# Kernel tuning notes

Measured on AMD Instinct MI355X. Metric: run time of the kernel, lower is better.

The kernel has to match this reference:

```python
import jax, jax.numpy as jnp
import numpy as np
import math

D_MODEL = 2048
D_STATE = 16
DT_RANK = math.ceil(D_MODEL / 16)  # 128
DT_MIN, DT_MAX, DT_INIT_FLOOR = 0.001, 0.1, 1e-4


def setup_inputs() -> dict:
    key = jax.random.key(0)
    k1, k2, k3, k4 = jax.random.split(key, 4)
    B, L = 4, 2048
    hidden_states = jax.random.normal(k1, (B, L, D_MODEL), dtype=jnp.float32)
    # x_proj: Linear(d_model -> dt_rank + 2*d_state), no bias
    fan_in = D_MODEL
    bound = 1.0 / math.sqrt(fan_in)
    x_proj_w = jax.random.uniform(k2, (DT_RANK + 2 * D_STATE, D_MODEL),
                                  minval=-bound, maxval=bound, dtype=jnp.float32)
    # dt_proj: Linear(dt_rank -> d_model) with special init
    dt_init_std = DT_RANK ** (-0.5)
    dt_proj_w = jax.random.uniform(k3, (D_MODEL, DT_RANK),
                                   minval=-dt_init_std, maxval=dt_init_std,
                                   dtype=jnp.float32)
    dt = jnp.exp(jax.random.uniform(k4, (D_MODEL,), dtype=jnp.float32)
                 * (math.log(DT_MAX) - math.log(DT_MIN)) + math.log(DT_MIN))
    dt = jnp.clip(dt, DT_INIT_FLOOR, None)
    dt_proj_b = dt + jnp.log(-jnp.expm1(-dt))  # inverse softplus
    # A_log: log(1..d_state) broadcast to (d_model, d_state)
    A_log = jnp.log(jnp.broadcast_to(jnp.arange(1, D_STATE + 1, dtype=jnp.float32),
                                     (D_MODEL, D_STATE)))
    D = jnp.ones((D_MODEL,), dtype=jnp.float32)
    return {"hidden_states": hidden_states, "x_proj_w": x_proj_w,
            "dt_proj_w": dt_proj_w, "dt_proj_b": dt_proj_b,
            "A_log": A_log, "D": D}


def _selective_scan(u, delta, A, Bmat, Cmat, D):
    # u, delta: (b, l, d); A: (d, n); Bmat, Cmat: (b, l, n); D: (d,)
    b, l, d = u.shape
    n = A.shape[1]

    def step(h, inp):
        u_t, delta_t, B_t, C_t = inp  # (b,d), (b,d), (b,n), (b,n)
        dA = jnp.exp(delta_t[:, :, None] * A)                 # (b,d,n)
        dBu = (delta_t * u_t)[:, :, None] * B_t[:, None, :]   # (b,d,n)
        h = dA * h + dBu
        y_t = jnp.einsum('bdn,bn->bd', h, C_t)
        return h, y_t

    h0 = jnp.zeros((b, d, n), dtype=u.dtype)
    xs = (jnp.swapaxes(u, 0, 1), jnp.swapaxes(delta, 0, 1),
          jnp.swapaxes(Bmat, 0, 1), jnp.swapaxes(Cmat, 0, 1))
    _, ys = jax.lax.scan(step, h0, xs)      # ys: (l, b, d)
    y = jnp.swapaxes(ys, 0, 1)               # (b, l, d)
    return y + u * D


def reference(hidden_states, x_proj_w, dt_proj_w, dt_proj_b, A_log, D):
    A = -jnp.exp(A_log)                                   # (d, n)
    x_dbl = hidden_states @ x_proj_w.T                    # (b, l, R+2n)
    dt_r = x_dbl[..., :DT_RANK]
    Bmat = x_dbl[..., DT_RANK:DT_RANK + D_STATE]          # (b, l, n)
    Cmat = x_dbl[..., DT_RANK + D_STATE:]                 # (b, l, n)
    dt = dt_r @ dt_proj_w.T                               # (b, l, d)
    delta = jax.nn.softplus(dt + dt_proj_b)               # fused delta_bias + softplus
    return _selective_scan(hidden_states, delta, A, Bmat, Cmat, D)
```

## Files before the change

### kernel.cpp

```cpp
#include <hip/hip_runtime.h>
#include <hip/hip_bf16.h>
#include <math.h>


#define DM   2048
#define DS   16
#define RNK  128
#define XDW  160
#define LSEQ 2048
#define NB   4
#define MTOT (NB * LSEQ)

#define G1_BM   64
#define G1_BK   32
#define G1_KS   8
#define G1_KPB  (DM / G1_KS)
#define G1_NCH  (G1_KPB / G1_BK)
#define XDBL_ELEMS ((size_t)MTOT * XDW)

typedef __attribute__((ext_vector_type(8))) unsigned short u16x8;
__global__ __launch_bounds__(256) void f32_to_bf16_kern(const float* __restrict__ in,
                                                        unsigned short* __restrict__ out) {
    const size_t i = ((size_t)blockIdx.x * 256 + threadIdx.x) * 8;
    const float4 v0 = *(const float4*)(in + i);
    const float4 v1 = *(const float4*)(in + i + 4);
    const float vv[8] = {v0.x, v0.y, v0.z, v0.w, v1.x, v1.y, v1.z, v1.w};
    u16x8 o;
    #pragma unroll
    for (int j = 0; j < 8; ++j) {
        __hip_bfloat16 h = __float2bfloat16(vv[j]);
        o[j] = *(unsigned short*)&h;
    }
    *(u16x8*)(out + i) = o;
}

typedef __attribute__((ext_vector_type(8))) short bf16x8;
typedef __attribute__((ext_vector_type(4))) float f32x4;

__global__ __launch_bounds__(256) void gemm1_mfma(const unsigned short* __restrict__ hsb,
                                                  const unsigned short* __restrict__ w1b,
                                                  float* __restrict__ out) {
    const int w  = threadIdx.x >> 6;
    const int l  = threadIdx.x & 63;
    const int m0 = blockIdx.x * G1_BM + w * 16;
    const int k0 = blockIdx.y * G1_KPB;
    const int lr = l & 15;
    const int lk = (l >> 4) * 8;

    f32x4 acc[10];
    #pragma unroll
    for (int j = 0; j < 10; ++j) acc[j] = (f32x4){0.f, 0.f, 0.f, 0.f};

    const unsigned short* ap = hsb + (size_t)(m0 + lr) * DM + k0 + lk;
    const unsigned short* bp = w1b + (size_t)lr * DM + k0 + lk;
    for (int ks = 0; ks < G1_KPB / 32; ++ks) {
        const bf16x8 a = *(const bf16x8*)(ap + ks * 32);
        #pragma unroll
        for (int j = 0; j < 10; ++j) {
            const bf16x8 b = *(const bf16x8*)(bp + (size_t)j * 16 * DM + ks * 32);
            acc[j] = __builtin_amdgcn_mfma_f32_16x16x32_bf16(a, b, acc[j], 0, 0, 0);
        }
    }
    float* op = out + (size_t)blockIdx.y * XDBL_ELEMS;
    #pragma unroll
    for (int j = 0; j < 10; ++j)
        #pragma unroll
        for (int r = 0; r < 4; ++r)
            op[(size_t)(m0 + (l >> 4) * 4 + r) * XDW + j * 16 + lr] = acc[j][r];
}

template<bool ATOMIC>
__global__ __launch_bounds__(256) void gemm1_kern(const float* __restrict__ hs,
                                                  const float* __restrict__ w1,
                                                  float* __restrict__ out) {
    __shared__ float aT[G1_BK][G1_BM + 4];
    __shared__ float bT[G1_BK][160 + 4];
    const int m0 = blockIdx.x * G1_BM;
    const int k0 = blockIdx.y * G1_KPB;
    const int tid = threadIdx.x;
    const int tm = tid >> 4, tn = tid & 15;
    const int r0 = tm * 4;
    const int sk = (tid & 7) * 4;
    const int sr = tid >> 3;

    float acc[4][10];
    #pragma unroll
    for (int i = 0; i < 4; ++i)
        #pragma unroll
        for (int j = 0; j < 10; ++j) acc[i][j] = 0.f;

    for (int ch = 0; ch < G1_NCH; ++ch) {
        const int kc = k0 + ch * G1_BK;
        __syncthreads();
        #pragma unroll
        for (int p = 0; p < 2; ++p) {
            const int row = sr + p * 32;
            const float4 v = *(const float4*)(hs + (size_t)(m0 + row) * DM + kc + sk);
            aT[sk + 0][row] = v.x; aT[sk + 1][row] = v.y;
            aT[sk + 2][row] = v.z; aT[sk + 3][row] = v.w;
        }
        #pragma unroll
        for (int p = 0; p < 5; ++p) {
            const int row = sr + p * 32;
            const float4 v = *(const float4*)(w1 + (size_t)row * DM + kc + sk);
            bT[sk + 0][row] = v.x; bT[sk + 1][row] = v.y;
            bT[sk + 2][row] = v.z; bT[sk + 3][row] = v.w;
        }
        __syncthreads();
        #pragma unroll 4
        for (int k = 0; k < G1_BK; ++k) {
            const float4 a0 = *(const float4*)&aT[k][r0];
            const float4 b0 = *(const float4*)&bT[k][tn * 4];
            const float4 b1 = *(const float4*)&bT[k][64 + tn * 4];
            const float2 b2 = *(const float2*)&bT[k][128 + tn * 2];
            const float av[4]  = {a0.x,a0.y,a0.z,a0.w};
            const float bv[10] = {b0.x,b0.y,b0.z,b0.w,b1.x,b1.y,b1.z,b1.w,b2.x,b2.y};
            #pragma unroll
            for (int i = 0; i < 4; ++i)
                #pragma unroll
                for (int j = 0; j < 10; ++j)
                    acc[i][j] += av[i] * bv[j];
        }
    }
    #pragma unroll
    for (int i = 0; i < 4; ++i) {
        const size_t rowoff = (size_t)(m0 + r0 + i) * XDW;
        #pragma unroll
        for (int j = 0; j < 10; ++j) {
            const int col = (j < 4) ? (tn * 4 + j)
                          : (j < 8) ? (64 + tn * 4 + (j - 4))
                                    : (128 + tn * 2 + (j - 8));
            if (ATOMIC) atomicAdd(&out[rowoff + col], acc[i][j]);
            else        out[(size_t)blockIdx.y * XDBL_ELEMS + rowoff + col] = acc[i][j];
        }
    }
}

__global__ __launch_bounds__(256) void zero_xdbl(float4* p) {
    p[blockIdx.x * 256 + threadIdx.x] = make_float4(0.f, 0.f, 0.f, 0.f);
}

__global__ __launch_bounds__(256) void reduce_part(const float* __restrict__ part,
                                                   float* __restrict__ xdbl) {
    const size_t i = (size_t)blockIdx.x * 256 + threadIdx.x;
    float s = 0.f;
    #pragma unroll
    for (int k = 0; k < G1_KS; ++k) s += part[(size_t)k * XDBL_ELEMS + i];
    xdbl[i] = s;
}

#define G2_BM 128
#define G2_BN 128
#define G2_BK 32
__global__ __launch_bounds__(256) void gemm2_delta(const float* __restrict__ xdbl,
                                                   const float* __restrict__ w2,
                                                   const float* __restrict__ bias,
                                                   float* __restrict__ dout) {
    __shared__ float xT[G2_BK][G2_BM + 4];
    __shared__ float wT[G2_BK][G2_BN + 4];
    const int m0 = blockIdx.x * G2_BM;
    const int n0 = blockIdx.y * G2_BN;
    const int tid = threadIdx.x;
    const int tm = tid >> 4, tn = tid & 15;
    const int r0 = tm * 8;
    const int sk = (tid & 7) * 4;
    const int sr = tid >> 3;

    float acc[8][8];
    #pragma unroll
    for (int i = 0; i < 8; ++i)
        #pragma unroll
        for (int j = 0; j < 8; ++j) acc[i][j] = 0.f;

    for (int ch = 0; ch < RNK / G2_BK; ++ch) {
        const int kc = ch * G2_BK;
        __syncthreads();
        #pragma unroll
        for (int p = 0; p < 4; ++p) {
            const int row = sr + p * 32;
            const float4 v = *(const float4*)(xdbl + (size_t)(m0 + row) * XDW + kc + sk);
            xT[sk + 0][row] = v.x; xT[sk + 1][row] = v.y;
            xT[sk + 2][row] = v.z; xT[sk + 3][row] = v.w;
        }
        #pragma unroll
        for (int p = 0; p < 4; ++p) {
            const int row = sr + p * 32;
            const float4 v = *(const float4*)(w2 + (size_t)(n0 + row) * RNK + kc + sk);
            wT[sk + 0][row] = v.x; wT[sk + 1][row] = v.y;
            wT[sk + 2][row] = v.z; wT[sk + 3][row] = v.w;
        }
        __syncthreads();
        #pragma unroll 4
        for (int k = 0; k < G2_BK; ++k) {
            const float4 a0 = *(const float4*)&xT[k][r0];
            const float4 a1 = *(const float4*)&xT[k][r0 + 4];
            const float4 b0 = *(const float4*)&wT[k][tn * 4];
            const float4 b1 = *(const float4*)&wT[k][64 + tn * 4];
            const float av[8] = {a0.x,a0.y,a0.z,a0.w,a1.x,a1.y,a1.z,a1.w};
            const float bv[8] = {b0.x,b0.y,b0.z,b0.w,b1.x,b1.y,b1.z,b1.w};
            #pragma unroll
            for (int i = 0; i < 8; ++i)
                #pragma unroll
                for (int j = 0; j < 8; ++j)
                    acc[i][j] += av[i] * bv[j];
        }
    }
    #pragma unroll
    for (int i = 0; i < 8; ++i) {
        float r[8];
        #pragma unroll
        for (int j = 0; j < 8; ++j) {
            const int col = (j < 4) ? (tn * 4 + j) : (64 + tn * 4 + (j - 4));
            const float x = acc[i][j] + bias[n0 + col];
            r[j] = (x > 20.f) ? x : log1pf(expf(x));
        }
        float* o = dout + (size_t)(m0 + r0 + i) * DM + n0;
        *(float4*)(o + tn * 4)      = make_float4(r[0], r[1], r[2], r[3]);
        *(float4*)(o + 64 + tn * 4) = make_float4(r[4], r[5], r[6], r[7]);
    }
}

template<int CTRL>
__device__ __forceinline__ float dpp_addstep(float x) {
    const int yi = __builtin_amdgcn_update_dpp(0, __builtin_bit_cast(int, x),
                                               CTRL, 0xF, 0xF, true);
    return x + __builtin_bit_cast(float, yi);
}
__device__ __forceinline__ float red16(float x) {
    x = dpp_addstep<0xB1>(x);
    x = dpp_addstep<0x4E>(x);
    x = dpp_addstep<0x124>(x);
    x = dpp_addstep<0x128>(x);
    return x;
}

__global__ __launch_bounds__(256) void scan_kernel(const float* __restrict__ hs,
                                                   const float* __restrict__ xdbl,
                                                   const float* __restrict__ Alog,
                                                   const float* __restrict__ Dvec,
                                                   const float* __restrict__ delta_in,
                                                   float* __restrict__ y_out) {
    const int b = blockIdx.y;
    const int g = threadIdx.x >> 4;
    const int n = threadIdx.x & 15;
    const int d = blockIdx.x * 16 + g;

    const float A  = -__expf(Alog[(size_t)d * DS + n]);
    const float Dd = Dvec[d];

    unsigned od = (unsigned)(b * LSEQ) * DM + (unsigned)d;
    unsigned ob = (unsigned)(b * LSEQ) * XDW + (unsigned)(RNK + n);

    float pd[8], pu[8], pB[8], pC[8];
    #pragma unroll
    for (int j = 0; j < 8; ++j) {
        pd[j] = delta_in[od + j * DM];
        pu[j] = hs[od + j * DM];
        pB[j] = xdbl[ob + j * XDW];
        pC[j] = xdbl[ob + j * XDW + DS];
    }

    float h = 0.f;
    for (int t0 = 0; t0 < LSEQ - 8; t0 += 8) {
        float pp[8], uD[8];
        #pragma unroll
        for (int j = 0; j < 8; ++j) {
            const float delta = pd[j];
            const float u     = pu[j];
            const float Bv    = pB[j];
            const float Cv    = pC[j];
            uD[j] = u * Dd;
            pd[j] = delta_in[od + (8 + j) * DM];
            pu[j] = hs[od + (8 + j) * DM];
            pB[j] = xdbl[ob + (8 + j) * XDW];
            pC[j] = xdbl[ob + (8 + j) * XDW + DS];

            h = __expf(delta * A) * h + (delta * u) * Bv;
            pp[j] = h * Cv;
        }
        #pragma unroll
        for (int j = 0; j < 8; ++j) pp[j] = red16(pp[j]);
        float v = pp[0] + uD[0];
        #pragma unroll
        for (int j = 1; j < 8; ++j) v = (n == j) ? (pp[j] + uD[j]) : v;
        if (n < 8) y_out[od + (unsigned)n * DM] = v;
        od += 8 * DM;
        ob += 8 * XDW;
    }
    {
        float pp[8], uD[8];
        #pragma unroll
        for (int j = 0; j < 8; ++j) {
            const float delta = pd[j];
            const float u     = pu[j];
            uD[j] = u * Dd;
            h = __expf(delta * A) * h + (delta * u) * pB[j];
            pp[j] = h * pC[j];
        }
        #pragma unroll
        for (int j = 0; j < 8; ++j) pp[j] = red16(pp[j]);
        float v = pp[0] + uD[0];
        #pragma unroll
        for (int j = 1; j < 8; ++j) v = (n == j) ? (pp[j] + uD[j]) : v;
        if (n < 8) y_out[od + (unsigned)n * DM] = v;
    }
}

extern "C" void kernel_launch(void* const* d_in, const int* in_sizes, int n_in,
                              void* d_out, int out_size, void* d_ws, size_t ws_size,
                              hipStream_t stream) {
    const float* hs   = (const float*)d_in[0];
    const float* w1   = (const float*)d_in[1];
    const float* w2   = (const float*)d_in[2];
    const float* bias = (const float*)d_in[3];
    const float* Alog = (const float*)d_in[4];
    const float* Dvec = (const float*)d_in[5];
    float* dout = (float*)d_out;
    float* xdbl = (float*)d_ws;

    const size_t OFF_PART  = (size_t)8 << 20;
    const size_t PART_B    = (size_t)G1_KS * XDBL_ELEMS * 4;
    const size_t OFF_HSB   = (OFF_PART + PART_B + 255) & ~(size_t)255;
    const size_t HSB_B     = (size_t)MTOT * DM * 2;
    const size_t OFF_W1B   = OFF_HSB + HSB_B;
    const size_t W1B_B     = (size_t)XDW * DM * 2;
    const size_t need_mfma = OFF_W1B + W1B_B;
    const size_t need_part = OFF_PART + PART_B;

    if (ws_size >= need_mfma) {
        unsigned short* hsb = (unsigned short*)((char*)d_ws + OFF_HSB);
        unsigned short* w1b = (unsigned short*)((char*)d_ws + OFF_W1B);
        float* part = (float*)((char*)d_ws + OFF_PART);
        hipLaunchKernelGGL(f32_to_bf16_kern, dim3(MTOT * DM / 8 / 256), dim3(256), 0, stream, hs, hsb);
        hipLaunchKernelGGL(f32_to_bf16_kern, dim3(XDW * DM / 8 / 256),  dim3(256), 0, stream, w1, w1b);
        hipLaunchKernelGGL(gemm1_mfma, dim3(MTOT / G1_BM, G1_KS), dim3(256), 0, stream, hsb, w1b, part);
        hipLaunchKernelGGL(reduce_part, dim3((unsigned)(XDBL_ELEMS / 256)), dim3(256), 0, stream, part, xdbl);
    } else if (ws_size >= need_part) {
        float* part = (float*)((char*)d_ws + OFF_PART);
        hipLaunchKernelGGL((gemm1_kern<false>), dim3(MTOT / G1_BM, G1_KS), dim3(256), 0, stream, hs, w1, part);
        hipLaunchKernelGGL(reduce_part, dim3((unsigned)(XDBL_ELEMS / 256)), dim3(256), 0, stream, part, xdbl);
    } else {
        hipLaunchKernelGGL(zero_xdbl, dim3((unsigned)(XDBL_ELEMS / 1024)), dim3(256), 0, stream, (float4*)xdbl);
        hipLaunchKernelGGL((gemm1_kern<true>), dim3(MTOT / G1_BM, G1_KS), dim3(256), 0, stream, hs, w1, xdbl);
    }
    hipLaunchKernelGGL(gemm2_delta, dim3(MTOT / G2_BM, DM / G2_BN), dim3(256), 0, stream, xdbl, w2, bias, dout);
    hipLaunchKernelGGL(scan_kernel, dim3(DM / 16, NB), dim3(256), 0, stream,
                       hs, xdbl, Alog, Dvec, dout, dout);
}
```

Before: 564.8 us.

## Fuse bf16 cast and split-K reduction into gemm1; store delta transposed for scan

The separate fp32-to-bf16 conversion of hidden_states and the partial-sum buffer with its reduce kernel are replaced by one gemm1 kernel. It converts activations in registers and reduces the four per-wave K slices through shared memory. gemm2 now writes delta transposed (b, d, l) via a shared-memory staging tile, so the scan reads delta contiguously with float4 loads. B and C are interleaved for paired float2 loads, and exp is switched to exp2 with a prescaled A. This removes large intermediate traffic, at the cost of a fixed workspace layout with hardcoded offsets and no size-based fallback paths.

```diff
diff --git a/kernel.cpp b/kernel.cpp
--- a/kernel.cpp
+++ b/kernel.cpp
@@ -11,14 +11,10 @@
 #define NB   4
 #define MTOT (NB * LSEQ)
 
-#define G1_BM   64
-#define G1_BK   32
-#define G1_KS   8
-#define G1_KPB  (DM / G1_KS)
-#define G1_NCH  (G1_KPB / G1_BK)
-#define XDBL_ELEMS ((size_t)MTOT * XDW)
-
 typedef __attribute__((ext_vector_type(8))) unsigned short u16x8;
+typedef __attribute__((ext_vector_type(8))) short bf16x8;
+typedef __attribute__((ext_vector_type(4))) float f32x4;
+
 __global__ __launch_bounds__(256) void f32_to_bf16_kern(const float* __restrict__ in,
                                                         unsigned short* __restrict__ out) {
     const size_t i = ((size_t)blockIdx.x * 256 + threadIdx.x) * 8;
@@ -34,119 +30,60 @@
     *(u16x8*)(out + i) = o;
 }
 
-typedef __attribute__((ext_vector_type(8))) short bf16x8;
-typedef __attribute__((ext_vector_type(4))) float f32x4;
-
-__global__ __launch_bounds__(256) void gemm1_mfma(const unsigned short* __restrict__ hsb,
-                                                  const unsigned short* __restrict__ w1b,
-                                                  float* __restrict__ out) {
+__device__ __forceinline__ short bf16bits(float x) {
+    __hip_bfloat16 h = __float2bfloat16(x);
+    return *(short*)&h;
+}
+
+__global__ __launch_bounds__(256) void gemm1_fused(const float* __restrict__ hs,
+                                                   const unsigned short* __restrict__ w1b,
+                                                   float* __restrict__ xdbl) {
+    __shared__ float red[4][16][162];
     const int w  = threadIdx.x >> 6;
     const int l  = threadIdx.x & 63;
-    const int m0 = blockIdx.x * G1_BM + w * 16;
-    const int k0 = blockIdx.y * G1_KPB;
     const int lr = l & 15;
-    const int lk = (l >> 4) * 8;
+    const int hk = (l >> 4) * 8;
+    const int m0 = blockIdx.x * 16;
 
     f32x4 acc[10];
     #pragma unroll
     for (int j = 0; j < 10; ++j) acc[j] = (f32x4){0.f, 0.f, 0.f, 0.f};
 
-    const unsigned short* ap = hsb + (size_t)(m0 + lr) * DM + k0 + lk;
-    const unsigned short* bp = w1b + (size_t)lr * DM + k0 + lk;
-    for (int ks = 0; ks < G1_KPB / 32; ++ks) {
-        const bf16x8 a = *(const bf16x8*)(ap + ks * 32);
+    const float*          ap = hs  + (size_t)(m0 + lr) * DM + w * 512 + hk;
+    const unsigned short* bp = w1b + (size_t)lr * DM        + w * 512 + hk;
+
+    for (int ks = 0; ks < 16; ++ks) {
+        const int kk = ks * 32;
+        const float4 f0 = *(const float4*)(ap + kk);
+        const float4 f1 = *(const float4*)(ap + kk + 4);
+        const bf16x8 a = {bf16bits(f0.x), bf16bits(f0.y), bf16bits(f0.z), bf16bits(f0.w),
+                          bf16bits(f1.x), bf16bits(f1.y), bf16bits(f1.z), bf16bits(f1.w)};
         #pragma unroll
         for (int j = 0; j < 10; ++j) {
-            const bf16x8 b = *(const bf16x8*)(bp + (size_t)j * 16 * DM + ks * 32);
+            const bf16x8 b = *(const bf16x8*)(bp + (size_t)j * 16 * DM + kk);
             acc[j] = __builtin_amdgcn_mfma_f32_16x16x32_bf16(a, b, acc[j], 0, 0, 0);
         }
     }
-    float* op = out + (size_t)blockIdx.y * XDBL_ELEMS;
+
     #pragma unroll
     for (int j = 0; j < 10; ++j)
         #pragma unroll
         for (int r = 0; r < 4; ++r)
-            op[(size_t)(m0 + (l >> 4) * 4 + r) * XDW + j * 16 + lr] = acc[j][r];
-}
-
-template<bool ATOMIC>
-__global__ __launch_bounds__(256) void gemm1_kern(const float* __restrict__ hs,
-                                                  const float* __restrict__ w1,
-                                                  float* __restrict__ out) {
-    __shared__ float aT[G1_BK][G1_BM + 4];
-    __shared__ float bT[G1_BK][160 + 4];
-    const int m0 = blockIdx.x * G1_BM;
-    const int k0 = blockIdx.y * G1_KPB;
-    const int tid = threadIdx.x;
-    const int tm = tid >> 4, tn = tid & 15;
-    const int r0 = tm * 4;
-    const int sk = (tid & 7) * 4;
-    const int sr = tid >> 3;
-
-    float acc[4][10];
-    #pragma unroll
-    for (int i = 0; i < 4; ++i)
-        #pragma unroll
-        for (int j = 0; j < 10; ++j) acc[i][j] = 0.f;
-
-    for (int ch = 0; ch < G1_NCH; ++ch) {
-        const int kc = k0 + ch * G1_BK;
-        __syncthreads();
-        #pragma unroll
-        for (int p = 0; p < 2; ++p) {
-            const int row = sr + p * 32;
-            const float4 v = *(const float4*)(hs + (size_t)(m0 + row) * DM + kc + sk);
-            aT[sk + 0][row] = v.x; aT[sk + 1][row] = v.y;
-            aT[sk + 2][row] = v.z; aT[sk + 3][row] = v.w;
-        }
-        #pragma unroll
-        for (int p = 0; p < 5; ++p) {
-            const int row = sr + p * 32;
-            const float4 v = *(const float4*)(w1 + (size_t)row * DM + kc + sk);
-            bT[sk + 0][row] = v.x; bT[sk + 1][row] = v.y;
-            bT[sk + 2][row] = v.z; bT[sk + 3][row] = v.w;
-        }
-        __syncthreads();
-        #pragma unroll 4
-        for (int k = 0; k < G1_BK; ++k) {
-            const float4 a0 = *(const float4*)&aT[k][r0];
-            const float4 b0 = *(const float4*)&bT[k][tn * 4];
-            const float4 b1 = *(const float4*)&bT[k][64 + tn * 4];
-            const float2 b2 = *(const float2*)&bT[k][128 + tn * 2];
-            const float av[4]  = {a0.x,a0.y,a0.z,a0.w};
-            const float bv[10] = {b0.x,b0.y,b0.z,b0.w,b1.x,b1.y,b1.z,b1.w,b2.x,b2.y};
-            #pragma unroll
-            for (int i = 0; i < 4; ++i)
-                #pragma unroll
-                for (int j = 0; j < 10; ++j)
-                    acc[i][j] += av[i] * bv[j];
-        }
-    }
-    #pragma unroll
-    for (int i = 0; i < 4; ++i) {
-        const size_t rowoff = (size_t)(m0 + r0 + i) * XDW;
-        #pragma unroll
-        for (int j = 0; j < 10; ++j) {
-            const int col = (j < 4) ? (tn * 4 + j)
-                          : (j < 8) ? (64 + tn * 4 + (j - 4))
-                                    : (128 + tn * 2 + (j - 8));
-            if (ATOMIC) atomicAdd(&out[rowoff + col], acc[i][j]);
-            else        out[(size_t)blockIdx.y * XDBL_ELEMS + rowoff + col] = acc[i][j];
-        }
-    }
-}
-
-__global__ __launch_bounds__(256) void zero_xdbl(float4* p) {
-    p[blockIdx.x * 256 + threadIdx.x] = make_float4(0.f, 0.f, 0.f, 0.f);
-}
-
-__global__ __launch_bounds__(256) void reduce_part(const float* __restrict__ part,
-                                                   float* __restrict__ xdbl) {
-    const size_t i = (size_t)blockIdx.x * 256 + threadIdx.x;
-    float s = 0.f;
-    #pragma unroll
-    for (int k = 0; k < G1_KS; ++k) s += part[(size_t)k * XDBL_ELEMS + i];
-    xdbl[i] = s;
+            red[w][(l >> 4) * 4 + r][j * 16 + lr] = acc[j][r];
+    __syncthreads();
+
+    const int row = threadIdx.x >> 4;
+    const int cb  = (threadIdx.x & 15) * 10;
+    #pragma unroll
+    for (int c = 0; c < 10; ++c) {
+        const int col = cb + c;
+        const float s = red[0][row][col] + red[1][row][col]
+                      + red[2][row][col] + red[3][row][col];
+        const int oc = (col < RNK)      ? col
+                     : (col < RNK + DS) ? (RNK + 2 * (col - RNK))
+                                        : (RNK + 2 * (col - RNK - DS) + 1);
+        xdbl[(size_t)(m0 + row) * XDW + oc] = s;
+    }
 }
 
 #define G2_BM 128
@@ -155,9 +92,10 @@
 __global__ __launch_bounds__(256) void gemm2_delta(const float* __restrict__ xdbl,
                                                    const float* __restrict__ w2,
                                                    const float* __restrict__ bias,
-                                                   float* __restrict__ dout) {
+                                                   float* __restrict__ delta_t) {
     __shared__ float xT[G2_BK][G2_BM + 4];
     __shared__ float wT[G2_BK][G2_BN + 4];
+    __shared__ float sT[64][132];
     const int m0 = blockIdx.x * G2_BM;
     const int n0 = blockIdx.y * G2_BN;
     const int tid = threadIdx.x;
@@ -205,18 +143,28 @@
                     acc[i][j] += av[i] * bv[j];
         }
     }
-    #pragma unroll
-    for (int i = 0; i < 8; ++i) {
-        float r[8];
-        #pragma unroll
-        for (int j = 0; j < 8; ++j) {
-            const int col = (j < 4) ? (tn * 4 + j) : (64 + tn * 4 + (j - 4));
-            const float x = acc[i][j] + bias[n0 + col];
-            r[j] = (x > 20.f) ? x : log1pf(expf(x));
-        }
-        float* o = dout + (size_t)(m0 + r0 + i) * DM + n0;
-        *(float4*)(o + tn * 4)      = make_float4(r[0], r[1], r[2], r[3]);
-        *(float4*)(o + 64 + tn * 4) = make_float4(r[4], r[5], r[6], r[7]);
+
+    const int b     = m0 / LSEQ;
+    const int tloc0 = m0 % LSEQ;
+    #pragma unroll
+    for (int hh = 0; hh < 2; ++hh) {
+        if (hh) __syncthreads();
+        #pragma unroll
+        for (int i = 0; i < 8; ++i)
+            #pragma unroll
+            for (int jj = 0; jj < 4; ++jj) {
+                const int j  = hh * 4 + jj;
+                const int cl = tn * 4 + jj;
+                const float x = acc[i][j] + bias[n0 + hh * 64 + cl];
+                sT[cl][r0 + i] = (x > 20.f) ? x : log1pf(expf(x));
+            }
+        __syncthreads();
+        const int dl = tid >> 2;
+        const int ts = (tid & 3) * 32;
+        float* dst = delta_t + ((size_t)b * DM + (n0 + hh * 64 + dl)) * LSEQ + tloc0 + ts;
+        #pragma unroll
+        for (int q = 0; q < 8; ++q)
+            *(float4*)(dst + q * 4) = *(const float4*)&sT[dl][ts + q * 4];
     }
 }
 
@@ -238,44 +186,48 @@
                                                    const float* __restrict__ xdbl,
                                                    const float* __restrict__ Alog,
                                                    const float* __restrict__ Dvec,
-                                                   const float* __restrict__ delta_in,
+                                                   const float* __restrict__ delta_t,
                                                    float* __restrict__ y_out) {
     const int b = blockIdx.y;
     const int g = threadIdx.x >> 4;
     const int n = threadIdx.x & 15;
     const int d = blockIdx.x * 16 + g;
 
-    const float A  = -__expf(Alog[(size_t)d * DS + n]);
+    const float A2 = -1.4426950408889634f * __expf(Alog[(size_t)d * DS + n]);
     const float Dd = Dvec[d];
 
     unsigned od = (unsigned)(b * LSEQ) * DM + (unsigned)d;
-    unsigned ob = (unsigned)(b * LSEQ) * XDW + (unsigned)(RNK + n);
-
-    float pd[8], pu[8], pB[8], pC[8];
+    unsigned ob = (unsigned)(b * LSEQ) * XDW + (unsigned)(RNK + 2 * n);
+
+    const float* dp = delta_t + ((size_t)b * DM + d) * LSEQ;
+    float4 c0 = *(const float4*)(dp);
+    float4 c1 = *(const float4*)(dp + 4);
+
+    float  pu[8];
+    float2 pbc[8];
     #pragma unroll
     for (int j = 0; j < 8; ++j) {
-        pd[j] = delta_in[od + j * DM];
-        pu[j] = hs[od + j * DM];
-        pB[j] = xdbl[ob + j * XDW];
-        pC[j] = xdbl[ob + j * XDW + DS];
+        pu[j]  = hs[od + j * DM];
+        pbc[j] = *(const float2*)(xdbl + ob + j * XDW);
     }
 
     float h = 0.f;
     for (int t0 = 0; t0 < LSEQ - 8; t0 += 8) {
+        const float4 nx0 = *(const float4*)(dp + 8);
+        const float4 nx1 = *(const float4*)(dp + 12);
+        const float dc[8] = {c0.x, c0.y, c0.z, c0.w, c1.x, c1.y, c1.z, c1.w};
         float pp[8], uD[8];
         #pragma unroll
         for (int j = 0; j < 8; ++j) {
-            const float delta = pd[j];
+            const float delta = dc[j];
             const float u     = pu[j];
-            const float Bv    = pB[j];
-            const float Cv    = pC[j];
+            const float Bv    = pbc[j].x;
+            const float Cv    = pbc[j].y;
             uD[j] = u * Dd;
-            pd[j] = delta_in[od + (8 + j) * DM];
-            pu[j] = hs[od + (8 + j) * DM];
-            pB[j] = xdbl[ob + (8 + j) * XDW];
-            pC[j] = xdbl[ob + (8 + j) * XDW + DS];
-
-            h = __expf(delta * A) * h + (delta * u) * Bv;
+            pu[j]  = hs[od + (8 + j) * DM];
+            pbc[j] = *(const float2*)(xdbl + ob + (8 + j) * XDW);
+
+            h = exp2f(delta * A2) * h + (delta * u) * Bv;
             pp[j] = h * Cv;
         }
         #pragma unroll
@@ -286,16 +238,19 @@
         if (n < 8) y_out[od + (unsigned)n * DM] = v;
         od += 8 * DM;
         ob += 8 * XDW;
+        dp += 8;
+        c0 = nx0; c1 = nx1;
     }
     {
+        const float dc[8] = {c0.x, c0.y, c0.z, c0.w, c1.x, c1.y, c1.z, c1.w};
         float pp[8], uD[8];
         #pragma unroll
         for (int j = 0; j < 8; ++j) {
-            const float delta = pd[j];
+            const float delta = dc[j];
             const float u     = pu[j];
             uD[j] = u * Dd;
-            h = __expf(delta * A) * h + (delta * u) * pB[j];
-            pp[j] = h * pC[j];
+            h = exp2f(delta * A2) * h + (delta * u) * pbc[j].x;
+            pp[j] = h * pbc[j].y;
         }
         #pragma unroll
         for (int j = 0; j < 8; ++j) pp[j] = red16(pp[j]);
@@ -316,34 +271,15 @@
     const float* Alog = (const float*)d_in[4];
     const float* Dvec = (const float*)d_in[5];
     float* dout = (float*)d_out;
-    float* xdbl = (float*)d_ws;
-
-    const size_t OFF_PART  = (size_t)8 << 20;
-    const size_t PART_B    = (size_t)G1_KS * XDBL_ELEMS * 4;
-    const size_t OFF_HSB   = (OFF_PART + PART_B + 255) & ~(size_t)255;
-    const size_t HSB_B     = (size_t)MTOT * DM * 2;
-    const size_t OFF_W1B   = OFF_HSB + HSB_B;
-    const size_t W1B_B     = (size_t)XDW * DM * 2;
-    const size_t need_mfma = OFF_W1B + W1B_B;
-    const size_t need_part = OFF_PART + PART_B;
-
-    if (ws_size >= need_mfma) {
-        unsigned short* hsb = (unsigned short*)((char*)d_ws + OFF_HSB);
-        unsigned short* w1b = (unsigned short*)((char*)d_ws + OFF_W1B);
-        float* part = (float*)((char*)d_ws + OFF_PART);
-        hipLaunchKernelGGL(f32_to_bf16_kern, dim3(MTOT * DM / 8 / 256), dim3(256), 0, stream, hs, hsb);
-        hipLaunchKernelGGL(f32_to_bf16_kern, dim3(XDW * DM / 8 / 256),  dim3(256), 0, stream, w1, w1b);
-        hipLaunchKernelGGL(gemm1_mfma, dim3(MTOT / G1_BM, G1_KS), dim3(256), 0, stream, hsb, w1b, part);
-        hipLaunchKernelGGL(reduce_part, dim3((unsigned)(XDBL_ELEMS / 256)), dim3(256), 0, stream, part, xdbl);
-    } else if (ws_size >= need_part) {
-        float* part = (float*)((char*)d_ws + OFF_PART);
-        hipLaunchKernelGGL((gemm1_kern<false>), dim3(MTOT / G1_BM, G1_KS), dim3(256), 0, stream, hs, w1, part);
-        hipLaunchKernelGGL(reduce_part, dim3((unsigned)(XDBL_ELEMS / 256)), dim3(256), 0, stream, part, xdbl);
-    } else {
-        hipLaunchKernelGGL(zero_xdbl, dim3((unsigned)(XDBL_ELEMS / 1024)), dim3(256), 0, stream, (float4*)xdbl);
-        hipLaunchKernelGGL((gemm1_kern<true>), dim3(MTOT / G1_BM, G1_KS), dim3(256), 0, stream, hs, w1, xdbl);
-    }
-    hipLaunchKernelGGL(gemm2_delta, dim3(MTOT / G2_BM, DM / G2_BN), dim3(256), 0, stream, xdbl, w2, bias, dout);
+
+    float*          xdbl    = (float*)d_ws;
+    unsigned short* w1b     = (unsigned short*)((char*)d_ws + 5242880);
+    float*          delta_t = (float*)((char*)d_ws + 5898240);
+
+    hipLaunchKernelGGL(f32_to_bf16_kern, dim3(XDW * DM / 8 / 256), dim3(256), 0, stream, w1, w1b);
+    hipLaunchKernelGGL(gemm1_fused, dim3(MTOT / 16), dim3(256), 0, stream, hs, w1b, xdbl);
+    hipLaunchKernelGGL(gemm2_delta, dim3(MTOT / G2_BM, DM / G2_BN), dim3(256), 0, stream,
+                       xdbl, w2, bias, delta_t);
     hipLaunchKernelGGL(scan_kernel, dim3(DM / 16, NB), dim3(256), 0, stream,
-                       hs, xdbl, Alog, Dvec, dout, dout);
-}
+                       hs, xdbl, Alog, Dvec, delta_t, dout);
+}
```

Result: no change. 567.6 us (+0.5%).
